# Optimization experiments

Hardware: AMD Instinct MI355X
Metric: run time of the kernel (lower is better)

The kernel has to match this reference:

```python
import jax, jax.numpy as jnp
import numpy as np

EPS = 1e-5


def _bn(h, gamma, beta):
    # BatchNorm1d, training mode: biased batch statistics over nodes
    mu = jnp.mean(h, axis=0)
    var = jnp.mean(jnp.square(h - mu), axis=0)
    return (h - mu) * jax.lax.rsqrt(var + EPS) * gamma + beta


def setup_inputs() -> dict:
    key = jax.random.key(0)
    ks = jax.random.split(key, 12)
    N, E, D, H = 50000, 800000, 128, 256
    x = jax.random.normal(ks[0], (N, D), dtype=jnp.float32)
    edge_index = jax.random.randint(ks[1], (2, E), 0, N, dtype=jnp.int64)
    train_node_id = jax.random.randint(ks[2], (10000,), 0, N, dtype=jnp.int64)
    def lin(k, fan_in, fan_out):
        bound = 1.0 / np.sqrt(fan_in)
        return jax.random.uniform(k, (fan_in, fan_out), jnp.float32, -bound, bound)
    return {
        "x": x, "edge_index": edge_index, "train_node_id": train_node_id,
        "W1": lin(ks[3], D, H), "b1": jnp.zeros((H,), jnp.float32),
        "W2": lin(ks[4], H, H), "b2": jnp.zeros((H,), jnp.float32),
        "W3": lin(ks[5], H, H), "b3": jnp.zeros((H,), jnp.float32),
        "g1": jnp.ones((H,), jnp.float32), "be1": jnp.zeros((H,), jnp.float32),
        "g2": jnp.ones((H,), jnp.float32), "be2": jnp.zeros((H,), jnp.float32),
        "g3": jnp.ones((H,), jnp.float32), "be3": jnp.zeros((H,), jnp.float32),
        "Wl": lin(ks[6], H, H), "bl": jnp.zeros((H,), jnp.float32),
        "Wf": lin(ks[7], H, 1), "bf": jnp.zeros((1,), jnp.float32),
    }


def reference(x, edge_index, train_node_id, W1, b1, W2, b2, W3, b3,
              g1, be1, g2, be2, g3, be3, Wl, bl, Wf, bf):
    N = x.shape[0]
    loops = jnp.arange(N, dtype=edge_index.dtype)
    row = jnp.concatenate([edge_index[0], loops])  # destinations
    col = jnp.concatenate([edge_index[1], loops])  # sources
    deg = jax.ops.segment_sum(jnp.ones_like(row, dtype=x.dtype), row, num_segments=N)
    d_isqrt = jax.lax.rsqrt(deg)  # deg >= 1 due to self loops
    norm = (d_isqrt[row] * d_isqrt[col])[:, None]  # [E+N, 1]

    def gcn(h, W, b):
        hW = h @ W
        agg = jax.ops.segment_sum(hW[col] * norm, row, num_segments=N)
        return agg + b

    h = jax.nn.relu(_bn(gcn(x, W1, b1), g1, be1))
    h = jax.nn.relu(_bn(gcn(h, W2, b2), g2, be2))
    h = jax.nn.relu(_bn(gcn(h, W3, b3), g3, be3))
    h = jax.nn.relu(h @ Wl + bl)
    h = h[train_node_id]
    return jnp.squeeze(h @ Wf + bf, -1)
```

## Files before the change

### kernel.cpp

```cpp
#include <hip/hip_runtime.h>

typedef unsigned short u16;
typedef __attribute__((ext_vector_type(8))) short short8;
typedef __attribute__((ext_vector_type(4))) float f32x4;

#define GPB 25

#define DEVFN static __device__ __forceinline__

DEVFN float b2f(u16 u) {
    union { float f; unsigned v; } x; x.v = ((unsigned)u) << 16; return x.f;
}
DEVFN u16 f2b(float f) {
    union { float f; unsigned v; } x; x.f = f;
    unsigned r = x.v + 0x7fffu + ((x.v >> 16) & 1u);
    return (u16)(r >> 16);
}

DEVFN int detect64(const int* __restrict__ p) {
    int orv = 0;
#pragma unroll
    for (int i = 1; i < 64; i += 2) orv |= p[i];
    return (orv == 0) ? 1 : 0;
}

DEVFN void accum_row8(short8 v, float* acc) {
    const unsigned* u = (const unsigned*)&v;
#pragma unroll
    for (int k = 0; k < 4; k++) {
        union { float f; unsigned w; } lo, hi;
        lo.w = u[k] << 16;
        hi.w = u[k] & 0xffff0000u;
        acc[2 * k] += lo.f;
        acc[2 * k + 1] += hi.f;
    }
}

__global__ void k_init(const float* __restrict__ W1, const float* __restrict__ W2,
                       const float* __restrict__ W3, const float* __restrict__ Wl,
                       u16* __restrict__ T1, u16* __restrict__ T2,
                       u16* __restrict__ T3, u16* __restrict__ Tl,
                       int* __restrict__ cnt, float* __restrict__ stat,
                       float* __restrict__ out, int N, int M) {
    int t = blockIdx.x * 256 + threadIdx.x;
    if (t < 229376) {
        const float* W; u16* T; int K; int idx;
        if (t < 32768)        { W = W1; T = T1; K = 128; idx = t; }
        else if (t < 98304)   { W = W2; T = T2; K = 256; idx = t - 32768; }
        else if (t < 163840)  { W = W3; T = T3; K = 256; idx = t - 98304; }
        else                  { W = Wl; T = Tl; K = 256; idx = t - 163840; }
        int k = idx >> 8, n = idx & 255;
        T[(size_t)n * K + k] = f2b(W[(size_t)k * 256 + n]);
    } else if (t < 229376 + N) {
        cnt[t - 229376] = 0;
    } else if (t < 229376 + N + 1536) {
        stat[t - 229376 - N] = 0.0f;
    } else if (t < 229376 + N + 1536 + M) {
        out[t - 229376 - N - 1536] = 0.0f;
    }
}

__global__ void k_fillb(const int* __restrict__ ei, int* __restrict__ cnt,
                        u16* __restrict__ slots, u16* __restrict__ ovf, int E) {
    int fl = detect64(ei);
    int t = blockIdx.x * 256 + threadIdx.x;
    int e0 = t * 2;
    if (e0 >= E) return;
    int r0, r1, c0, c1;
    bool two = (e0 + 1 < E);
    if (fl) {
        const int4* p4 = (const int4*)ei;
        int4 d = p4[t];
        int4 s = p4[(E >> 1) + t];
        r0 = d.x; r1 = d.z; c0 = s.x; c1 = s.z;
    } else {
        const int2* p2 = (const int2*)ei;
        int2 d = p2[t];
        int2 s = p2[(E >> 1) + t];
        r0 = d.x; r1 = d.y; c0 = s.x; c1 = s.y;
    }
    int p0 = atomicAdd(&cnt[r0], 1);
    if (p0 < 32)      slots[(size_t)r0 * 32 + p0] = (u16)c0;
    else if (p0 < 96) ovf[(size_t)r0 * 64 + (p0 - 32)] = (u16)c0;
    if (two) {
        int p1 = atomicAdd(&cnt[r1], 1);
        if (p1 < 32)      slots[(size_t)r1 * 32 + p1] = (u16)c1;
        else if (p1 < 96) ovf[(size_t)r1 * 64 + (p1 - 32)] = (u16)c1;
    }
}

__global__ void k_cvtx(const float* __restrict__ x, const int* __restrict__ cnt,
                       float* __restrict__ disq, u16* __restrict__ xb, int N) {
    int t = blockIdx.x * 256 + threadIdx.x;
    if (t >= N * 32) return;
    int row = t >> 5;
    int f0 = (t & 31) * 4;
    float d = rsqrtf((float)(cnt[row] + 1));
    if ((t & 31) == 0) disq[row] = d;
    float4 v = *(const float4*)(x + (size_t)row * 128 + f0);
    ushort4 o;
    o.x = f2b(v.x * d); o.y = f2b(v.y * d); o.z = f2b(v.z * d); o.w = f2b(v.w * d);
    *(ushort4*)(xb + (size_t)(f0 >> 5) * N * 32 + (size_t)row * 32 + (f0 & 31)) = o;
}


template<int PBITS>
__global__ __launch_bounds__(256) void k_gatherP(
        const u16* __restrict__ src, const int* __restrict__ cnt,
        const u16* __restrict__ slots, const u16* __restrict__ ovf,
        const float* __restrict__ disq, u16* __restrict__ dst, int N) {
    const int NP = 1 << PBITS;
    const size_t N32 = (size_t)N * 32;
    int plane = blockIdx.x & (NP - 1);
    int lane = threadIdx.x & 63;
    int wv = threadIdx.x >> 6;
    int j = lane >> 2;
    int piece = lane & 3;
    int dbase = (blockIdx.x >> PBITS) * 64 + wv * 16;
    int d = dbase + j;
    bool live = d < N;
    int e = live ? min(cnt[d], 95) : -1;
    float di = live ? disq[d] : 0.f;

    short8 sb = *(const short8*)(slots + (size_t)dbase * 32 + lane * 8);
    const unsigned* sbw = (const unsigned*)&sb;

    const u16* sbase = src + (size_t)plane * N32 + piece * 8;
    const u16* ov = ovf + (size_t)d * 64;

    float acc[8] = {0.f, 0.f, 0.f, 0.f, 0.f, 0.f, 0.f, 0.f};

    int m = e;
    m = max(m, __shfl_xor(m, 4, 64));
    m = max(m, __shfl_xor(m, 8, 64));
    m = max(m, __shfl_xor(m, 16, 64));
    m = max(m, __shfl_xor(m, 32, 64));

    int mm = min(m, 31);
    for (int rb = 0; rb < 4; rb++) {
        int r0 = rb * 8;
        if (r0 > mm) break;
        int srcl = j * 4 + rb;
        int cs[8];
#pragma unroll
        for (int rw = 0; rw < 4; rw++) {
            unsigned w = (unsigned)__shfl((int)sbw[rw], srcl, 64);
#pragma unroll
            for (int hh = 0; hh < 2; hh++) {
                int r = r0 + rw * 2 + hh;
                u16 s = hh ? (u16)(w >> 16) : (u16)(w & 0xffffu);
                int c = -1;
                if (r < e) c = (int)s;
                else if (r == e) c = d;
                cs[rw * 2 + hh] = c;
            }
        }
        short8 vs[8];
#pragma unroll
        for (int k = 0; k < 8; k++)
            if (cs[k] >= 0) vs[k] = *(const short8*)(sbase + (size_t)cs[k] * 32);
#pragma unroll
        for (int k = 0; k < 8; k++)
            if (cs[k] >= 0) accum_row8(vs[k], acc);
    }
    if (m >= 32) {
        for (int r = 32; r <= m; r++) {
            int c = -1;
            if (r < e) c = (int)ov[r - 32];
            else if (r == e) c = d;
            if (c >= 0) {
                short8 v = *(const short8*)(sbase + (size_t)c * 32);
                accum_row8(v, acc);
            }
        }
    }
    if (live) {
        short8 o;
        u16* op = (u16*)&o;
#pragma unroll
        for (int k = 0; k < 8; k++) op[k] = f2b(acc[k] * di);
        __builtin_nontemporal_store(o,
            (short8*)(dst + (size_t)plane * N32 + (size_t)d * 32 + piece * 8));
    }
}


template<int KS>
__global__ __launch_bounds__(256, 2) void k_gemm_rb(
        const u16* __restrict__ A, const u16* __restrict__ Wt,
        float* __restrict__ Cf, int PS, int Gtot,
        float* __restrict__ stat, const float* __restrict__ bias,
        const float* __restrict__ Wfp, const float* __restrict__ bfp,
        float* __restrict__ outp) {
    constexpr int K = KS * 32;
    __shared__ float sbuf[4][2][64];
    int wv = threadIdx.x >> 6;
    int lane = threadIdx.x & 63;
    int quad = lane >> 4;
    int mr = lane & 15;
    int colbase = blockIdx.y * 64;
    int g0 = blockIdx.x * GPB;

    short8 Bf[4][KS];
#pragma unroll
    for (int j = 0; j < 4; j++)
#pragma unroll
        for (int s = 0; s < KS; s++)
            Bf[j][s] = *(const short8*)(Wt + (size_t)(colbase + j * 16 + mr) * K + s * 32 + quad * 8);

    float4 bv4[4], wf4[4];
    if (Wfp) {
#pragma unroll
        for (int j = 0; j < 4; j++) {
            bv4[j] = *(const float4*)(bias + colbase + j * 16 + quad * 4);
            wf4[j] = *(const float4*)(Wfp + colbase + j * 16 + quad * 4);
        }
    }

    f32x4 sreg[4], s2reg[4];
#pragma unroll
    for (int j = 0; j < 4; j++) {
        sreg[j] = (f32x4){0.f, 0.f, 0.f, 0.f};
        s2reg[j] = (f32x4){0.f, 0.f, 0.f, 0.f};
    }

    for (int g = wv; g < GPB; g += 4) {
        int gg = g0 + g;
        if (gg >= Gtot) continue;
        int row = gg * 16 + mr;
        const u16* Ap = A + (size_t)row * 32 + quad * 8;

        short8 Af[KS];
#pragma unroll
        for (int s = 0; s < KS; s++) Af[s] = *(const short8*)(Ap + (size_t)s * PS);

        f32x4 acc[4];
#pragma unroll
        for (int j = 0; j < 4; j++) acc[j] = (f32x4){0.f, 0.f, 0.f, 0.f};
#pragma unroll
        for (int s = 0; s < KS; s++)
#pragma unroll
            for (int j = 0; j < 4; j++)
                acc[j] = __builtin_amdgcn_mfma_f32_16x16x32_bf16(Bf[j][s], Af[s], acc[j], 0, 0, 0);

        if (Wfp) {
            float pr = 0.f;
#pragma unroll
            for (int j = 0; j < 4; j++) {
                const float* bj = (const float*)&bv4[j];
                const float* wj = (const float*)&wf4[j];
#pragma unroll
                for (int r = 0; r < 4; r++) {
                    float v = fmaxf(acc[j][r] + bj[r], 0.f);
                    pr += v * wj[r];
                }
            }
            pr += __shfl_xor(pr, 16, 64);
            pr += __shfl_xor(pr, 32, 64);
            if (quad == 0) {
                float v = pr;
                if (blockIdx.y == 0) v += bfp[0];
                atomicAdd(&outp[row], v);
            }
            continue;
        }

        float* cp = Cf + (size_t)row * 256 + colbase + quad * 4;
#pragma unroll
        for (int j = 0; j < 4; j++) {
            *(f32x4*)(cp + j * 16) = acc[j];
            sreg[j] += acc[j];
            s2reg[j] += acc[j] * acc[j];
        }
    }

    if (stat) {
#pragma unroll
        for (int j = 0; j < 4; j++) {
#pragma unroll
            for (int r = 0; r < 4; r++) {
                float a = sreg[j][r], b = s2reg[j][r];
                a += __shfl_xor(a, 1, 64); b += __shfl_xor(b, 1, 64);
                a += __shfl_xor(a, 2, 64); b += __shfl_xor(b, 2, 64);
                a += __shfl_xor(a, 4, 64); b += __shfl_xor(b, 4, 64);
                a += __shfl_xor(a, 8, 64); b += __shfl_xor(b, 8, 64);
                if (mr == 0) {
                    sbuf[wv][0][j * 16 + quad * 4 + r] = a;
                    sbuf[wv][1][j * 16 + quad * 4 + r] = b;
                }
            }
        }
        __syncthreads();
        int t = threadIdx.x;
        if (t < 128) {
            int which = t >> 6, c = t & 63;
            float v = sbuf[0][which][c] + sbuf[1][which][c] +
                      sbuf[2][which][c] + sbuf[3][which][c];
            atomicAdd(&stat[which * 256 + colbase + c], v);
        }
    }
}


__global__ void k_bnapply(const float* __restrict__ t, const float* __restrict__ stat,
                          const float* __restrict__ gamma, const float* __restrict__ beta,
                          u16* __restrict__ h, int N, float invN,
                          const float* __restrict__ scale) {
    size_t tt = (size_t)blockIdx.x * 256 + threadIdx.x;
    size_t base = tt * 4;
    if (base >= (size_t)N * 256) return;
    int f0 = (int)(base & 255);
    int row = (int)(base >> 8);
    float sc2 = scale ? scale[row] : 1.0f;
    float4 v = *(const float4*)(t + base);
    float r[4] = {v.x, v.y, v.z, v.w};
    ushort4 o;
    u16* op = (u16*)&o;
#pragma unroll
    for (int j = 0; j < 4; j++) {
        int f = f0 + j;
        float mean = stat[f] * invN;
        float var = stat[256 + f] * invN - mean * mean;
        float rstd = rsqrtf(var + 1e-5f);
        float sc = rstd * gamma[f];
        float sh = beta[f] - mean * sc;
        op[j] = f2b(fmaxf(r[j] * sc + sh, 0.0f) * sc2);
    }
    *(ushort4*)(h + (size_t)(f0 >> 5) * N * 32 + (size_t)row * 32 + (f0 & 31)) = o;
}

__global__ void k_bnapply_idx(const float* __restrict__ t, const float* __restrict__ stat,
                              const float* __restrict__ gamma, const float* __restrict__ beta,
                              const int* __restrict__ idx, u16* __restrict__ zin,
                              int M, float invN) {
    int fl = detect64(idx);
    size_t tt = (size_t)blockIdx.x * 256 + threadIdx.x;
    size_t base = tt * 4;
    if (base >= (size_t)M * 256) return;
    int f0 = (int)(base & 255);
    int row = (int)(base >> 8);
    int node = idx[(size_t)row << fl];
    float4 v = *(const float4*)(t + (size_t)node * 256 + f0);
    float r[4] = {v.x, v.y, v.z, v.w};
    ushort4 o;
    u16* op = (u16*)&o;
#pragma unroll
    for (int j = 0; j < 4; j++) {
        int f = f0 + j;
        float mean = stat[f] * invN;
        float var = stat[256 + f] * invN - mean * mean;
        float rstd = rsqrtf(var + 1e-5f);
        float sc = rstd * gamma[f];
        float sh = beta[f] - mean * sc;
        op[j] = f2b(fmaxf(r[j] * sc + sh, 0.0f));
    }
    *(ushort4*)(zin + (size_t)(f0 >> 5) * M * 32 + (size_t)row * 32 + (f0 & 31)) = o;
}


extern "C" void kernel_launch(void* const* d_in, const int* in_sizes, int n_in,
                              void* d_out, int out_size, void* d_ws, size_t ws_size,
                              hipStream_t stream) {
    const int D = 128, H = 256;
    const int N = in_sizes[0] / D;
    const int E = in_sizes[1] / 2;
    const int M = in_sizes[2];

    const float* x = (const float*)d_in[0];
    const int* ei = (const int*)d_in[1];
    const int* tnid = (const int*)d_in[2];
    const float* W1 = (const float*)d_in[3];
    const float* W2 = (const float*)d_in[5];
    const float* W3 = (const float*)d_in[7];
    const float* g1 = (const float*)d_in[9];
    const float* be1 = (const float*)d_in[10];
    const float* g2 = (const float*)d_in[11];
    const float* be2 = (const float*)d_in[12];
    const float* g3 = (const float*)d_in[13];
    const float* be3 = (const float*)d_in[14];
    const float* Wl = (const float*)d_in[15];
    const float* bl = (const float*)d_in[16];
    const float* Wf = (const float*)d_in[17];
    const float* bfp = (const float*)d_in[18];
    float* out = (float*)d_out;

    char* w = (char*)d_ws;
    size_t off = 0;
    auto carve = [&](size_t bytes) -> void* {
        void* p = w + off;
        off = (off + bytes + 255) & ~(size_t)255;
        return p;
    };

    float* stat = (float*)carve(3 * 512 * 4);
    float* disq = (float*)carve((size_t)N * 4);
    int* cnt = (int*)carve((size_t)N * 4);
    u16* slots = (u16*)carve((size_t)N * 32 * 2);
    u16* ovf = (u16*)carve((size_t)N * 64 * 2);
    u16* Wt1 = (u16*)carve((size_t)H * D * 2);
    u16* Wt2 = (u16*)carve((size_t)H * H * 2);
    u16* Wt3 = (u16*)carve((size_t)H * H * 2);
    u16* Wtl = (u16*)carve((size_t)H * H * 2);
    u16* xb = (u16*)carve((size_t)N * D * 2);
    u16* aggx = (u16*)carve((size_t)N * D * 2);
    u16* aggh = (u16*)carve((size_t)N * H * 2);
    float* tb = (float*)carve((size_t)N * H * 4);
    u16* hb = (u16*)carve((size_t)N * H * 2);
    u16* zin = (u16*)carve((size_t)M * H * 2);

    const float invN = 1.0f / (float)N;

    const int Gn = N / 16;
    const int Gm = M / 16;
    dim3 gemm_grid((Gn + GPB - 1) / GPB, 4);
    dim3 gemm_grid_m((Gm + GPB - 1) / GPB, 4);
    const int PSn = N * 32;
    const int PSm = M * 32;
    const int chunks = (N + 63) / 64;
    const int PB = (int)(((size_t)N * H / 4 + 255) / 256);
    const int PBm = (int)(((size_t)M * H / 4 + 255) / 256);

    k_init<<<(229376 + N + 1536 + M + 255) / 256, 256, 0, stream>>>(
        W1, W2, W3, Wl, Wt1, Wt2, Wt3, Wtl, cnt, stat, out, N, M);
    k_fillb<<<(E / 2 + 255) / 256, 256, 0, stream>>>(ei, cnt, slots, ovf, E);
    k_cvtx<<<(N * 32 + 255) / 256, 256, 0, stream>>>(x, cnt, disq, xb, N);

    k_gatherP<2><<<4 * chunks, 256, 0, stream>>>(xb, cnt, slots, ovf, disq, aggx, N);
    k_gemm_rb<4><<<gemm_grid, 256, 0, stream>>>(aggx, Wt1, tb, PSn, Gn, stat, nullptr, nullptr, nullptr, nullptr);
    k_bnapply<<<PB, 256, 0, stream>>>(tb, stat, g1, be1, hb, N, invN, disq);
    k_gatherP<3><<<8 * chunks, 256, 0, stream>>>(hb, cnt, slots, ovf, disq, aggh, N);
    k_gemm_rb<8><<<gemm_grid, 256, 0, stream>>>(aggh, Wt2, tb, PSn, Gn, stat + 512, nullptr, nullptr, nullptr, nullptr);
    k_bnapply<<<PB, 256, 0, stream>>>(tb, stat + 512, g2, be2, hb, N, invN, disq);
    k_gatherP<3><<<8 * chunks, 256, 0, stream>>>(hb, cnt, slots, ovf, disq, aggh, N);
    k_gemm_rb<8><<<gemm_grid, 256, 0, stream>>>(aggh, Wt3, tb, PSn, Gn, stat + 1024, nullptr, nullptr, nullptr, nullptr);
    k_bnapply_idx<<<PBm, 256, 0, stream>>>(tb, stat + 1024, g3, be3, tnid, zin, M, invN);

    k_gemm_rb<8><<<gemm_grid_m, 256, 0, stream>>>(zin, Wtl, nullptr, PSm, Gm, nullptr, bl, Wf, bfp, out);
}
```

Baseline: 411.2 us.

## Shard edge-bucketing atomics per XCC and build packed CSR slots in prep

Edge bucketing now counts edges per destination in eight per-XCC counters using workgroup-scope atomics, with eight local slots per XCC. A new prep kernel compacts those slots into the 32-entry slot table and places the self-loop there, sending any spill to an atomic overflow list. The same kernel also does the degree-normalised x conversion that k_cvtx used to do. The gather then reads a packed count/total word and no longer needs special self-loop handling. The aim is less cross-die contention on the counter atomics, in exchange for an extra compaction pass and scratch buffers aliased onto hb and tb. It also relies on workgroup-scope atomics staying coherent within each XCC.

```diff
diff --git a/kernel.cpp b/kernel.cpp
--- a/kernel.cpp
+++ b/kernel.cpp
@@ -8,9 +8,6 @@
 
 #define DEVFN static __device__ __forceinline__
 
-DEVFN float b2f(u16 u) {
-    union { float f; unsigned v; } x; x.v = ((unsigned)u) << 16; return x.f;
-}
 DEVFN u16 f2b(float f) {
     union { float f; unsigned v; } x; x.f = f;
     unsigned r = x.v + 0x7fffu + ((x.v >> 16) & 1u);
@@ -22,6 +19,12 @@
 #pragma unroll
     for (int i = 1; i < 64; i += 2) orv |= p[i];
     return (orv == 0) ? 1 : 0;
+}
+
+DEVFN unsigned get_xcc() {
+    unsigned x;
+    asm volatile("s_getreg_b32 %0, hwreg(HW_REG_XCC_ID)" : "=s"(x));
+    return x & 7u;
 }
 
 DEVFN void accum_row8(short8 v, float* acc) {
@@ -40,9 +43,10 @@
                        const float* __restrict__ W3, const float* __restrict__ Wl,
                        u16* __restrict__ T1, u16* __restrict__ T2,
                        u16* __restrict__ T3, u16* __restrict__ Tl,
-                       int* __restrict__ cnt, float* __restrict__ stat,
-                       float* __restrict__ out, int N, int M) {
+                       int* __restrict__ z9,
+                       float* __restrict__ stat, float* __restrict__ out, int N, int M) {
     int t = blockIdx.x * 256 + threadIdx.x;
+    int Z = (N * 9) / 4;
     if (t < 229376) {
         const float* W; u16* T; int K; int idx;
         if (t < 32768)        { W = W1; T = T1; K = 128; idx = t; }
@@ -51,18 +55,22 @@
         else                  { W = Wl; T = Tl; K = 256; idx = t - 163840; }
         int k = idx >> 8, n = idx & 255;
         T[(size_t)n * K + k] = f2b(W[(size_t)k * 256 + n]);
-    } else if (t < 229376 + N) {
-        cnt[t - 229376] = 0;
-    } else if (t < 229376 + N + 1536) {
-        stat[t - 229376 - N] = 0.0f;
-    } else if (t < 229376 + N + 1536 + M) {
-        out[t - 229376 - N - 1536] = 0.0f;
-    }
-}
-
-__global__ void k_fillb(const int* __restrict__ ei, int* __restrict__ cnt,
-                        u16* __restrict__ slots, u16* __restrict__ ovf, int E) {
+    } else if (t < 229376 + Z) {
+        ((int4*)z9)[t - 229376] = (int4){0, 0, 0, 0};
+    } else if (t < 229376 + Z + 384) {
+        ((float4*)stat)[t - 229376 - Z] = (float4){0.f, 0.f, 0.f, 0.f};
+    } else if (t < 229376 + Z + 384 + (M + 3) / 4) {
+        int i = (t - 229376 - Z - 384) * 4;
+        if (i + 3 < M) *(float4*)(out + i) = (float4){0.f, 0.f, 0.f, 0.f};
+        else for (int k = i; k < M; k++) out[k] = 0.f;
+    }
+}
+
+__global__ void k_fillb(const int* __restrict__ ei, unsigned* __restrict__ cnt8,
+                        int* __restrict__ ovfc, u16* __restrict__ slots8,
+                        u16* __restrict__ ovf, int E) {
     int fl = detect64(ei);
+    unsigned xcc = get_xcc();
     int t = blockIdx.x * 256 + threadIdx.x;
     int e0 = t * 2;
     if (e0 >= E) return;
@@ -79,30 +87,86 @@
         int2 s = p2[(E >> 1) + t];
         r0 = d.x; r1 = d.y; c0 = s.x; c1 = s.y;
     }
-    int p0 = atomicAdd(&cnt[r0], 1);
-    if (p0 < 32)      slots[(size_t)r0 * 32 + p0] = (u16)c0;
-    else if (p0 < 96) ovf[(size_t)r0 * 64 + (p0 - 32)] = (u16)c0;
+    {
+        unsigned p = __hip_atomic_fetch_add(&cnt8[(size_t)r0 * 8 + xcc], 1u,
+                                            __ATOMIC_RELAXED, __HIP_MEMORY_SCOPE_WORKGROUP);
+        if (p < 8) slots8[(size_t)r0 * 64 + xcc * 8 + p] = (u16)c0;
+        else { int q = atomicAdd(&ovfc[r0], 1); if (q < 64) ovf[(size_t)r0 * 64 + q] = (u16)c0; }
+    }
     if (two) {
-        int p1 = atomicAdd(&cnt[r1], 1);
-        if (p1 < 32)      slots[(size_t)r1 * 32 + p1] = (u16)c1;
-        else if (p1 < 96) ovf[(size_t)r1 * 64 + (p1 - 32)] = (u16)c1;
-    }
-}
-
-__global__ void k_cvtx(const float* __restrict__ x, const int* __restrict__ cnt,
-                       float* __restrict__ disq, u16* __restrict__ xb, int N) {
-    int t = blockIdx.x * 256 + threadIdx.x;
-    if (t >= N * 32) return;
-    int row = t >> 5;
-    int f0 = (t & 31) * 4;
-    float d = rsqrtf((float)(cnt[row] + 1));
-    if ((t & 31) == 0) disq[row] = d;
-    float4 v = *(const float4*)(x + (size_t)row * 128 + f0);
-    ushort4 o;
-    o.x = f2b(v.x * d); o.y = f2b(v.y * d); o.z = f2b(v.z * d); o.w = f2b(v.w * d);
-    *(ushort4*)(xb + (size_t)(f0 >> 5) * N * 32 + (size_t)row * 32 + (f0 & 31)) = o;
-}
-
+        unsigned p = __hip_atomic_fetch_add(&cnt8[(size_t)r1 * 8 + xcc], 1u,
+                                            __ATOMIC_RELAXED, __HIP_MEMORY_SCOPE_WORKGROUP);
+        if (p < 8) slots8[(size_t)r1 * 64 + xcc * 8 + p] = (u16)c1;
+        else { int q = atomicAdd(&ovfc[r1], 1); if (q < 64) ovf[(size_t)r1 * 64 + q] = (u16)c1; }
+    }
+}
+
+__global__ __launch_bounds__(256) void k_prep(
+        const unsigned* __restrict__ cnt8, int* __restrict__ ovfc,
+        const u16* __restrict__ slots8, int* __restrict__ cnt,
+        u16* __restrict__ slots, u16* __restrict__ ovf,
+        const float* __restrict__ x, float* __restrict__ disq,
+        u16* __restrict__ xb, int N, int CB) {
+    int b = blockIdx.x;
+    if (b < CB) {
+        int lane = threadIdx.x & 63;
+        int wv = threadIdx.x >> 6;
+        int j = lane >> 2;
+        int p = lane & 3;
+        int d = b * 64 + wv * 16 + j;
+        bool valid = d < N;
+        int dd = valid ? d : (N - 1);
+        int2 c2 = *(const int2*)(cnt8 + (size_t)dd * 8 + p * 2);
+        int nA = min(c2.x, 8), nB = min(c2.y, 8);
+        int v = nA + nB;
+        int w = c2.x + c2.y;
+        int j4 = lane & ~3;
+        int v0 = __shfl(v, j4 + 0, 64);
+        int v1 = __shfl(v, j4 + 1, 64);
+        int v2 = __shfl(v, j4 + 2, 64);
+        int base = (p > 0 ? v0 : 0) + (p > 1 ? v1 : 0) + (p > 2 ? v2 : 0);
+        int wsum = w;
+        wsum += __shfl_xor(wsum, 1, 64);
+        wsum += __shfl_xor(wsum, 2, 64);
+        const u16* s8 = slots8 + (size_t)dd * 64 + p * 16;
+        u16* sd = slots + (size_t)dd * 32;
+        if (valid) {
+            for (int i = 0; i < nA; i++) {
+                int pos = base + i; u16 val = s8[i];
+                if (pos < 32) sd[pos] = val;
+                else { int q = atomicAdd(&ovfc[dd], 1); if (q < 64) ovf[(size_t)dd * 64 + q] = val; }
+            }
+            for (int i = 0; i < nB; i++) {
+                int pos = base + nA + i; u16 val = s8[8 + i];
+                if (pos < 32) sd[pos] = val;
+                else { int q = atomicAdd(&ovfc[dd], 1); if (q < 64) ovf[(size_t)dd * 64 + q] = val; }
+            }
+            if (p == 3) {
+                int selfpos = base + nA + nB;
+                if (selfpos < 32) sd[selfpos] = (u16)dd;
+                else { int q = atomicAdd(&ovfc[dd], 1); if (q < 64) ovf[(size_t)dd * 64 + q] = (u16)dd; }
+                int dc = min(selfpos + 1, 32);
+                int tot = min(wsum + 1, dc + 64);
+                cnt[dd] = dc | (tot << 8);
+            }
+        }
+    } else {
+        int tt = (b - CB) * 256 + threadIdx.x;
+        if (tt >= N * 32) return;
+        int row = tt >> 5;
+        int f0 = (tt & 31) * 4;
+        const unsigned* c8 = cnt8 + (size_t)row * 8;
+        unsigned s = 0;
+#pragma unroll
+        for (int k = 0; k < 8; k++) s += c8[k];
+        float dq = rsqrtf((float)(s + 1));
+        if ((tt & 31) == 0) disq[row] = dq;
+        float4 vx = *(const float4*)(x + (size_t)row * 128 + f0);
+        ushort4 o;
+        o.x = f2b(vx.x * dq); o.y = f2b(vx.y * dq); o.z = f2b(vx.z * dq); o.w = f2b(vx.w * dq);
+        *(ushort4*)(xb + (size_t)(f0 >> 5) * N * 32 + (size_t)row * 32 + (f0 & 31)) = o;
+    }
+}
 
 template<int PBITS>
 __global__ __launch_bounds__(256) void k_gatherP(
@@ -119,7 +183,9 @@
     int dbase = (blockIdx.x >> PBITS) * 64 + wv * 16;
     int d = dbase + j;
     bool live = d < N;
-    int e = live ? min(cnt[d], 95) : -1;
+    int packed = live ? cnt[d] : 0;
+    int dc = packed & 0xff;
+    int tot = packed >> 8;
     float di = live ? disq[d] : 0.f;
 
     short8 sb = *(const short8*)(slots + (size_t)dbase * 32 + lane * 8);
@@ -130,16 +196,15 @@
 
     float acc[8] = {0.f, 0.f, 0.f, 0.f, 0.f, 0.f, 0.f, 0.f};
 
-    int m = e;
+    int m = dc;
     m = max(m, __shfl_xor(m, 4, 64));
     m = max(m, __shfl_xor(m, 8, 64));
     m = max(m, __shfl_xor(m, 16, 64));
     m = max(m, __shfl_xor(m, 32, 64));
 
-    int mm = min(m, 31);
     for (int rb = 0; rb < 4; rb++) {
         int r0 = rb * 8;
-        if (r0 > mm) break;
+        if (r0 >= m) break;
         int srcl = j * 4 + rb;
         int cs[8];
 #pragma unroll
@@ -149,10 +214,7 @@
             for (int hh = 0; hh < 2; hh++) {
                 int r = r0 + rw * 2 + hh;
                 u16 s = hh ? (u16)(w >> 16) : (u16)(w & 0xffffu);
-                int c = -1;
-                if (r < e) c = (int)s;
-                else if (r == e) c = d;
-                cs[rw * 2 + hh] = c;
+                cs[rw * 2 + hh] = (r < dc) ? (int)s : -1;
             }
         }
         short8 vs[8];
@@ -163,17 +225,21 @@
         for (int k = 0; k < 8; k++)
             if (cs[k] >= 0) accum_row8(vs[k], acc);
     }
-    if (m >= 32) {
-        for (int r = 32; r <= m; r++) {
-            int c = -1;
-            if (r < e) c = (int)ov[r - 32];
-            else if (r == e) c = d;
-            if (c >= 0) {
-                short8 v = *(const short8*)(sbase + (size_t)c * 32);
-                accum_row8(v, acc);
-            }
-        }
-    }
+
+    int nov = tot - dc;
+    int novm = nov;
+    novm = max(novm, __shfl_xor(novm, 4, 64));
+    novm = max(novm, __shfl_xor(novm, 8, 64));
+    novm = max(novm, __shfl_xor(novm, 16, 64));
+    novm = max(novm, __shfl_xor(novm, 32, 64));
+    for (int r = 0; r < novm; r++) {
+        if (r < nov) {
+            int c = (int)ov[r];
+            short8 v = *(const short8*)(sbase + (size_t)c * 32);
+            accum_row8(v, acc);
+        }
+    }
+
     if (live) {
         short8 o;
         u16* op = (u16*)&o;
@@ -183,7 +249,6 @@
             (short8*)(dst + (size_t)plane * N32 + (size_t)d * 32 + piece * 8));
     }
 }
-
 
 template<int KS>
 __global__ __launch_bounds__(256, 2) void k_gemm_rb(
@@ -408,6 +473,10 @@
     u16* hb = (u16*)carve((size_t)N * H * 2);
     u16* zin = (u16*)carve((size_t)M * H * 2);
 
+    unsigned* cnt8 = (unsigned*)hb;
+    int* ovfc = (int*)(hb + (size_t)N * 8 * 2);
+    u16* slots8 = (u16*)tb;
+
     const float invN = 1.0f / (float)N;
 
     const int Gn = N / 16;
@@ -419,11 +488,14 @@
     const int chunks = (N + 63) / 64;
     const int PB = (int)(((size_t)N * H / 4 + 255) / 256);
     const int PBm = (int)(((size_t)M * H / 4 + 255) / 256);
-
-    k_init<<<(229376 + N + 1536 + M + 255) / 256, 256, 0, stream>>>(
-        W1, W2, W3, Wl, Wt1, Wt2, Wt3, Wtl, cnt, stat, out, N, M);
-    k_fillb<<<(E / 2 + 255) / 256, 256, 0, stream>>>(ei, cnt, slots, ovf, E);
-    k_cvtx<<<(N * 32 + 255) / 256, 256, 0, stream>>>(x, cnt, disq, xb, N);
+    const int CB = chunks;
+    const int XB = (N * 32 + 255) / 256;
+    const int initT = 229376 + (N * 9) / 4 + 384 + (M + 3) / 4;
+
+    k_init<<<(initT + 255) / 256, 256, 0, stream>>>(
+        W1, W2, W3, Wl, Wt1, Wt2, Wt3, Wtl, (int*)cnt8, stat, out, N, M);
+    k_fillb<<<(E / 2 + 255) / 256, 256, 0, stream>>>(ei, cnt8, ovfc, slots8, ovf, E);
+    k_prep<<<CB + XB, 256, 0, stream>>>(cnt8, ovfc, slots8, cnt, slots, ovf, x, disq, xb, N, CB);
 
     k_gatherP<2><<<4 * chunks, 256, 0, stream>>>(xb, cnt, slots, ovf, disq, aggx, N);
     k_gemm_rb<4><<<gemm_grid, 256, 0, stream>>>(aggx, Wt1, tb, PSn, Gn, stat, nullptr, nullptr, nullptr, nullptr);
```

Measured after the change: 416.0 us. About the same (+1.2%).
